# Kernel tuning notes

Measured on AMD Instinct MI355X. Metric: run time of the kernel, lower is better.

## Reference

```python
import jax, jax.numpy as jnp
import numpy as np

D_MODEL = 1024
NUM_HEADS = 16
HEAD_DIM = D_MODEL // NUM_HEADS


def setup_inputs() -> dict:
    key = jax.random.key(0)
    kx, kq, kk, kv, ko = jax.random.split(key, 5)
    B, T = 2, 2048
    scale = 1.0 / np.sqrt(D_MODEL)
    return {
        "x": jax.random.normal(kx, (B, T, D_MODEL), dtype=jnp.float32),
        "wq": jax.random.normal(kq, (D_MODEL, D_MODEL), dtype=jnp.float32) * scale,
        "wk": jax.random.normal(kk, (D_MODEL, D_MODEL), dtype=jnp.float32) * scale,
        "wv": jax.random.normal(kv, (D_MODEL, D_MODEL), dtype=jnp.float32) * scale,
        "wo": jax.random.normal(ko, (D_MODEL, D_MODEL), dtype=jnp.float32) * scale,
    }


def _split_heads(x):
    b, t, _ = x.shape
    return x.reshape(b, t, NUM_HEADS, HEAD_DIM).transpose(0, 2, 1, 3)  # [b,h,t,d]


def reference(x, wq, wk, wv, wo):
    q = _split_heads(x @ wq)
    k = _split_heads(x @ wk)
    v = _split_heads(x @ wv)
    inv_sqrt_d = jnp.asarray(1.0 / np.sqrt(HEAD_DIM), x.dtype)
    scores = jnp.einsum("bhqd,bhkd->bhqk", q, k) * inv_sqrt_d
    weights = jax.nn.softmax(scores, axis=-1)  # dropout rate 0.0 -> identity
    out = jnp.einsum("bhqk,bhkd->bhqd", weights, v)
    b, h, t, d = out.shape
    out = out.transpose(0, 2, 1, 3).reshape(b, t, D_MODEL)
    return out @ wo
```

## Files before the change

### kernel.cpp

```cpp
#include <hip/hip_runtime.h>
#include <stdint.h>

using bf16   = __bf16;
using bf16x8 = __bf16 __attribute__((ext_vector_type(8)));
using bf16x4 = __bf16 __attribute__((ext_vector_type(4)));
using f32x4  = float  __attribute__((ext_vector_type(4)));
using f32x16 = float  __attribute__((ext_vector_type(16)));
using u32x4  = uint32_t __attribute__((ext_vector_type(4)));

#define DM 1024
#define T_ 2048
#define NH 16

__device__ __forceinline__ void gl_lds16(const void* g, void* l) {
  __builtin_amdgcn_global_load_lds(
      (__attribute__((address_space(1))) void*)g,
      (__attribute__((address_space(3))) void*)l, 16, 0, 0);
}

__device__ __forceinline__ f32x4 mfma16(bf16x8 a, bf16x8 b, f32x4 c) {
  return __builtin_amdgcn_mfma_f32_16x16x32_bf16(a, b, c, 0, 0, 0);
}
__device__ __forceinline__ f32x16 mfma32(bf16x8 a, bf16x8 b, f32x16 c) {
  return __builtin_amdgcn_mfma_f32_32x32x16_bf16(a, b, c, 0, 0, 0);
}
__device__ __forceinline__ uint32_t cvtpk(float lo, float hi) {
  uint32_t r;
  asm volatile("v_cvt_pk_bf16_f32 %0, %1, %2" : "=v"(r) : "v"(lo), "v"(hi));
  return r;
}

__global__ __launch_bounds__(256)
void k_prep(const float* __restrict__ x,
            const float* __restrict__ w0, const float* __restrict__ w1,
            const float* __restrict__ w2, const float* __restrict__ w3,
            bf16* __restrict__ xb, bf16* __restrict__ wtq, bf16* __restrict__ wto) {
  __shared__ float tile[64][68];
  const int bid = blockIdx.x;
  if (bid < 2048) {
    const size_t i = (size_t)bid * 256 + threadIdx.x;
    const float4 a = *(const float4*)(x + i * 8);
    const float4 c = *(const float4*)(x + i * 8 + 4);
    bf16x8 v;
    v[0] = (bf16)a.x; v[1] = (bf16)a.y; v[2] = (bf16)a.z; v[3] = (bf16)a.w;
    v[4] = (bf16)c.x; v[5] = (bf16)c.y; v[6] = (bf16)c.z; v[7] = (bf16)c.w;
    *(bf16x8*)(xb + i * 8) = v;
    return;
  }
  const int wblk = bid - 2048;
  const int z = wblk >> 8;
  const int bx = wblk & 15, by = (wblk >> 4) & 15;
  const float* w = (z == 0) ? w0 : (z == 1) ? w1 : (z == 2) ? w2 : w3;
  bf16* wt = (z < 3) ? (wtq + (size_t)z * 1024 * 1024) : wto;
  const float scale = (z == 0) ? 0.125f * 1.44269504f : 1.0f;
  const int tx = threadIdx.x & 15;
  const int ty = threadIdx.x >> 4;
  const int k0 = by * 64, n0 = bx * 64;
#pragma unroll
  for (int j = 0; j < 4; ++j) {
    const int r = ty + 16 * j;
    const float4 v = *(const float4*)(w + (size_t)(k0 + r) * DM + n0 + tx * 4);
    tile[r][tx * 4 + 0] = v.x; tile[r][tx * 4 + 1] = v.y;
    tile[r][tx * 4 + 2] = v.z; tile[r][tx * 4 + 3] = v.w;
  }
  __syncthreads();
#pragma unroll
  for (int j = 0; j < 4; ++j) {
    const int r = ty + 16 * j;
    bf16x4 o;
    o[0] = (bf16)(tile[tx * 4 + 0][r] * scale);
    o[1] = (bf16)(tile[tx * 4 + 1][r] * scale);
    o[2] = (bf16)(tile[tx * 4 + 2][r] * scale);
    o[3] = (bf16)(tile[tx * 4 + 3][r] * scale);
    *(bf16x4*)(wt + (size_t)(n0 + r) * DM + k0 + tx * 4) = o;
  }
}

template<int MODE>
__global__ __launch_bounds__(256)
void k_gemm(const bf16* __restrict__ A, const bf16* __restrict__ BT,
            bf16* __restrict__ Qg, bf16* __restrict__ Kf, bf16* __restrict__ Vf,
            float* __restrict__ Cout) {
  constexpr int BN = (MODE == 0) ? 128 : 64;
  constexpr int NTW = BN / 32;
  constexpr int TNX = (MODE == 0) ? 3 : 2;
  __shared__ __align__(16) bf16 Ash[128 * 32];
  __shared__ __align__(16) bf16 Bsh[BN * 32];
  const int xcd = blockIdx.x & 7, idx = blockIdx.x >> 3;
  const int tn = xcd * TNX + idx % TNX;
  const int tm = idx / TNX;
  const int lane = threadIdx.x & 63, w = threadIdx.x >> 6;
  const int wm = w >> 1, wn = w & 1;
  const int r16 = lane & 15, g = lane >> 4;
  f32x4 acc[4][NTW] = {};
  const bf16* Arow = A + (size_t)tm * 128 * DM;
  const bf16* Brow = BT + (size_t)tn * BN * DM;
  for (int k0 = 0; k0 < DM; k0 += 32) {
#pragma unroll
    for (int t = 0; t < 2; ++t) {
      const int q = t * 256 + w * 64 + lane;
      gl_lds16(Arow + (size_t)(q >> 2) * DM + k0 + (q & 3) * 8, Ash + (t * 256 + w * 64) * 8);
    }
#pragma unroll
    for (int t = 0; t < BN / 64; ++t) {
      const int q = t * 256 + w * 64 + lane;
      gl_lds16(Brow + (size_t)(q >> 2) * DM + k0 + (q & 3) * 8, Bsh + (t * 256 + w * 64) * 8);
    }
    __syncthreads();
    bf16x8 af[4], bfr[NTW];
#pragma unroll
    for (int mt = 0; mt < 4; ++mt)
      af[mt] = *(const bf16x8*)(Ash + (wm * 64 + mt * 16 + r16) * 32 + g * 8);
#pragma unroll
    for (int nt = 0; nt < NTW; ++nt)
      bfr[nt] = *(const bf16x8*)(Bsh + (wn * (BN / 2) + nt * 16 + r16) * 32 + g * 8);
#pragma unroll
    for (int mt = 0; mt < 4; ++mt)
#pragma unroll
      for (int nt = 0; nt < NTW; ++nt)
        acc[mt][nt] = mfma16(af[mt], bfr[nt], acc[mt][nt]);
    __syncthreads();
  }
#pragma unroll
  for (int mt = 0; mt < 4; ++mt) {
#pragma unroll
    for (int nt = 0; nt < NTW; ++nt) {
      const int ncol = tn * BN + wn * (BN / 2) + nt * 16 + r16;
      const int m0 = tm * 128 + wm * 64 + mt * 16 + g * 4;
      if (MODE == 0) {
        const int which = ncol >> 10, nl = ncol & 1023;
        const int h = nl >> 6, d = nl & 63;
        const int b = m0 >> 11, t0 = m0 & 2047;
        const size_t hb = (size_t)(b * NH + h) * (T_ * 64);
        if (which == 2) {
          const int kt = t0 >> 6, s = (t0 & 63) >> 4, hi2 = (t0 >> 3) & 1, j0 = t0 & 7;
          const int dh = d >> 5, d31 = d & 31;
          bf16x4 pv;
#pragma unroll
          for (int r = 0; r < 4; ++r) pv[r] = (bf16)acc[mt][nt][r];
          *(bf16x4*)(Vf + hb + kt * 4096 + (s * 2 + dh) * 512 + (hi2 * 32 + d31) * 8 + j0) = pv;
        } else if (which == 1) {
          const int kt = t0 >> 6, kh2 = (t0 >> 5) & 1;
          const int s = d >> 4, hi2 = (d >> 3) & 1, j = d & 7;
          bf16* base = Kf + hb + kt * 4096 + (s * 2 + kh2) * 512 + hi2 * 256 + j;
#pragma unroll
          for (int r = 0; r < 4; ++r)
            base[((t0 & 31) + r) * 8] = (bf16)acc[mt][nt][r];
        } else {
#pragma unroll
          for (int r = 0; r < 4; ++r)
            Qg[hb + (size_t)(t0 + r) * 64 + d] = (bf16)acc[mt][nt][r];
        }
      } else {
#pragma unroll
        for (int r = 0; r < 4; ++r)
          Cout[(size_t)(m0 + r) * DM + ncol] = acc[mt][nt][r];
      }
    }
  }
}

__global__ __launch_bounds__(512)
void k_attn(const bf16* __restrict__ Qg, const bf16* __restrict__ Kf,
            const bf16* __restrict__ Vf, bf16* __restrict__ Ao) {
  __shared__ __align__(16) bf16 Ksh[2][2][64 * 64];
  __shared__ __align__(16) bf16 Vsh[2][2][64 * 64];
  __shared__ float Lsh[4][64];
  const int lin = ((blockIdx.x & 7) << 6) | (blockIdx.x >> 3);
  const int bh = lin >> 4, qt = lin & 15;
  const int lane = threadIdx.x & 63, w = threadIdx.x >> 6;
  const int qw = w & 3, kh = w >> 2;
  const int l31 = lane & 31, hi = lane >> 5;
  const bf16* Qb  = Qg + (size_t)bh * T_ * 64;
  const bf16* Kfh = Kf + (size_t)bh * T_ * 64;
  const bf16* Vfh = Vf + (size_t)bh * T_ * 64;
  const int q0 = qt * 128 + qw * 32;
  bf16x8 qb[4];
#pragma unroll
  for (int s = 0; s < 4; ++s)
    qb[s] = *(const bf16x8*)(Qb + (size_t)(q0 + l31) * 64 + s * 16 + hi * 8);
  f32x16 o0 = {}, o1 = {};
  float llocal = 0.f;

  auto stage = [&](int buf, int ti) {
#pragma unroll
    for (int j = 0; j < 2; ++j) {
      const int idx = qw * 2 + j;
      gl_lds16(Kfh + (size_t)ti * 4096 + idx * 512 + lane * 8, &Ksh[kh][buf][idx * 512]);
      gl_lds16(Vfh + (size_t)ti * 4096 + idx * 512 + lane * 8, &Vsh[kh][buf][idx * 512]);
    }
  };
  auto pvstep = [&](const f32x16& sv, int si, const bf16* Vc, int s) {
    uint32_t a0 = cvtpk(sv[si + 0], sv[si + 1]);
    uint32_t a1 = cvtpk(sv[si + 2], sv[si + 3]);
    uint32_t b0 = cvtpk(sv[si + 4], sv[si + 5]);
    uint32_t b1 = cvtpk(sv[si + 6], sv[si + 7]);
    asm volatile("v_permlane32_swap_b32 %0, %1" : "+v"(a0), "+v"(b0));
    asm volatile("v_permlane32_swap_b32 %0, %1" : "+v"(a1), "+v"(b1));
    u32x4 fr; fr[0] = a0; fr[1] = a1; fr[2] = b0; fr[3] = b1;
    const bf16x8 pas = __builtin_bit_cast(bf16x8, fr);
    const bf16x8 v0 = *(const bf16x8*)(Vc + (s * 2 + 0) * 512 + lane * 8);
    const bf16x8 v1 = *(const bf16x8*)(Vc + (s * 2 + 1) * 512 + lane * 8);
    o0 = mfma32(pas, v0, o0);
    o1 = mfma32(pas, v1, o1);
  };

  constexpr int NTH = T_ / 64 / 2;
  stage(0, kh * NTH);
  __syncthreads();
  for (int i = 0; i < NTH; ++i) {
    const int cur = i & 1;
    if (i + 1 < NTH) stage(cur ^ 1, kh * NTH + i + 1);
    const bf16* Kc = &Ksh[kh][cur][0];
    const bf16* Vc = &Vsh[kh][cur][0];
    f32x16 st0 = {}, st1 = {};
    __builtin_amdgcn_s_setprio(1);
#pragma unroll
    for (int s = 0; s < 4; ++s) {
      const bf16x8 k0 = *(const bf16x8*)(Kc + (s * 2 + 0) * 512 + lane * 8);
      st0 = mfma32(k0, qb[s], st0);
    }
#pragma unroll
    for (int s = 0; s < 4; ++s) {
      const bf16x8 k1 = *(const bf16x8*)(Kc + (s * 2 + 1) * 512 + lane * 8);
      st1 = mfma32(k1, qb[s], st1);
    }
    __builtin_amdgcn_s_setprio(0);
#pragma unroll
    for (int r = 0; r < 16; ++r) {
      st0[r] = __builtin_amdgcn_exp2f(st0[r]); llocal += st0[r];
    }
    __builtin_amdgcn_s_setprio(1);
    pvstep(st0, 0, Vc, 0);
    pvstep(st0, 8, Vc, 1);
    __builtin_amdgcn_s_setprio(0);
#pragma unroll
    for (int r = 0; r < 16; ++r) {
      st1[r] = __builtin_amdgcn_exp2f(st1[r]); llocal += st1[r];
    }
    __builtin_amdgcn_s_setprio(1);
    pvstep(st1, 0, Vc, 2);
    pvstep(st1, 8, Vc, 3);
    __builtin_amdgcn_s_setprio(0);
    __syncthreads();
  }
  float* cb = (float*)&Ksh[0][0][0] + qw * 2048;
  if (kh == 1) {
#pragma unroll
    for (int r = 0; r < 16; ++r) {
      cb[r * 64 + lane]        = o0[r];
      cb[(16 + r) * 64 + lane] = o1[r];
    }
    Lsh[qw][lane] = llocal;
  }
  __syncthreads();
  if (kh == 0) {
    llocal += Lsh[qw][lane];
#pragma unroll
    for (int r = 0; r < 16; ++r) {
      o0[r] += cb[r * 64 + lane];
      o1[r] += cb[(16 + r) * 64 + lane];
    }
    llocal += __shfl_xor(llocal, 32);
    const int b = bh >> 4, h = bh & 15;
#pragma unroll
    for (int r = 0; r < 16; ++r) {
      const int qoff = (r & 3) + 8 * (r >> 2) + 4 * hi;
      const float linv = 1.f / __shfl(llocal, qoff);
      const size_t base = ((size_t)(b * T_ + q0 + qoff)) * DM + h * 64 + l31;
      Ao[base]      = (bf16)(o0[r] * linv);
      Ao[base + 32] = (bf16)(o1[r] * linv);
    }
  }
}

extern "C" void kernel_launch(void* const* d_in, const int* in_sizes, int n_in,
                              void* d_out, int out_size, void* d_ws, size_t ws_size,
                              hipStream_t stream) {
  const float* x  = (const float*)d_in[0];
  const float* wq = (const float*)d_in[1];
  const float* wk = (const float*)d_in[2];
  const float* wv = (const float*)d_in[3];
  const float* wo = (const float*)d_in[4];
  char* ws = (char*)d_ws;
  const size_t MB = 1024 * 1024;
  bf16* xb   = (bf16*)(ws + 0);
  bf16* wtq  = (bf16*)(ws + 8 * MB);
  bf16* wto  = (bf16*)(ws + 14 * MB);
  bf16* Qg   = (bf16*)(ws + 16 * MB);
  bf16* Kfb  = (bf16*)(ws + 24 * MB);
  bf16* Vfb  = (bf16*)(ws + 32 * MB);

  k_prep<<<dim3(3072), dim3(256), 0, stream>>>(x, wq, wk, wv, wo, xb, wtq, wto);
  k_gemm<0><<<dim3(768), dim3(256), 0, stream>>>(xb, wtq, Qg, Kfb, Vfb, (float*)nullptr);
  k_attn<<<dim3(512), dim3(512), 0, stream>>>(Qg, Kfb, Vfb, xb);
  k_gemm<1><<<dim3(512), dim3(256), 0, stream>>>(xb, wto, (bf16*)nullptr, (bf16*)nullptr,
                                                 (bf16*)nullptr, (float*)d_out);
}
```

Before: 119.0 us.

## Double GEMM K-tile to 64 with XOR-swizzled LDS layout

After: 121.6 us. 2.1% more time.

```diff
diff --git a/kernel.cpp b/kernel.cpp
--- a/kernel.cpp
+++ b/kernel.cpp
@@ -84,41 +84,55 @@
   constexpr int BN = (MODE == 0) ? 128 : 64;
   constexpr int NTW = BN / 32;
   constexpr int TNX = (MODE == 0) ? 3 : 2;
-  __shared__ __align__(16) bf16 Ash[128 * 32];
-  __shared__ __align__(16) bf16 Bsh[BN * 32];
+  __shared__ __align__(16) bf16 Ash[128 * 64];
+  __shared__ __align__(16) bf16 Bsh[BN * 64];
   const int xcd = blockIdx.x & 7, idx = blockIdx.x >> 3;
   const int tn = xcd * TNX + idx % TNX;
   const int tm = idx / TNX;
   const int lane = threadIdx.x & 63, w = threadIdx.x >> 6;
   const int wm = w >> 1, wn = w & 1;
   const int r16 = lane & 15, g = lane >> 4;
+  const int srow8 = lane >> 3;
+  const int sch = (lane & 7) ^ srow8;
   f32x4 acc[4][NTW] = {};
   const bf16* Arow = A + (size_t)tm * 128 * DM;
   const bf16* Brow = BT + (size_t)tn * BN * DM;
-  for (int k0 = 0; k0 < DM; k0 += 32) {
-#pragma unroll
-    for (int t = 0; t < 2; ++t) {
-      const int q = t * 256 + w * 64 + lane;
-      gl_lds16(Arow + (size_t)(q >> 2) * DM + k0 + (q & 3) * 8, Ash + (t * 256 + w * 64) * 8);
-    }
-#pragma unroll
-    for (int t = 0; t < BN / 64; ++t) {
-      const int q = t * 256 + w * 64 + lane;
-      gl_lds16(Brow + (size_t)(q >> 2) * DM + k0 + (q & 3) * 8, Bsh + (t * 256 + w * 64) * 8);
+  for (int k0 = 0; k0 < DM; k0 += 64) {
+#pragma unroll
+    for (int j = 0; j < 4; ++j) {
+      const int rb = w * 32 + j * 8;
+      gl_lds16(Arow + (size_t)(rb + srow8) * DM + k0 + sch * 8, Ash + rb * 64);
+    }
+#pragma unroll
+    for (int j = 0; j < BN / 32; ++j) {
+      const int rb = w * (BN / 4) + j * 8;
+      gl_lds16(Brow + (size_t)(rb + srow8) * DM + k0 + sch * 8, Bsh + rb * 64);
     }
     __syncthreads();
-    bf16x8 af[4], bfr[NTW];
-#pragma unroll
-    for (int mt = 0; mt < 4; ++mt)
-      af[mt] = *(const bf16x8*)(Ash + (wm * 64 + mt * 16 + r16) * 32 + g * 8);
-#pragma unroll
-    for (int nt = 0; nt < NTW; ++nt)
-      bfr[nt] = *(const bf16x8*)(Bsh + (wn * (BN / 2) + nt * 16 + r16) * 32 + g * 8);
-#pragma unroll
-    for (int mt = 0; mt < 4; ++mt)
-#pragma unroll
-      for (int nt = 0; nt < NTW; ++nt)
-        acc[mt][nt] = mfma16(af[mt], bfr[nt], acc[mt][nt]);
+    bf16x8 af[4][2], bfr[NTW][2];
+#pragma unroll
+    for (int mt = 0; mt < 4; ++mt) {
+      const int R = wm * 64 + mt * 16 + r16;
+#pragma unroll
+      for (int kk = 0; kk < 2; ++kk)
+        af[mt][kk] = *(const bf16x8*)((const char*)Ash + R * 128 +
+                                      (((kk * 4 + g) ^ (R & 7)) << 4));
+    }
+#pragma unroll
+    for (int nt = 0; nt < NTW; ++nt) {
+      const int R = wn * (BN / 2) + nt * 16 + r16;
+#pragma unroll
+      for (int kk = 0; kk < 2; ++kk)
+        bfr[nt][kk] = *(const bf16x8*)((const char*)Bsh + R * 128 +
+                                       (((kk * 4 + g) ^ (R & 7)) << 4));
+    }
+#pragma unroll
+    for (int kk = 0; kk < 2; ++kk)
+#pragma unroll
+      for (int mt = 0; mt < 4; ++mt)
+#pragma unroll
+        for (int nt = 0; nt < NTW; ++nt)
+          acc[mt][nt] = mfma16(af[mt][kk], bfr[nt][kk], acc[mt][nt]);
     __syncthreads();
   }
 #pragma unroll
```

## Double-buffer GEMM LDS tiles and split softmax row-sum accumulators

Applied to the files above, without the earlier changes.

Result: slower. 124.3 us (+4.4%).

```diff
diff --git a/kernel.cpp b/kernel.cpp
--- a/kernel.cpp
+++ b/kernel.cpp
@@ -84,8 +84,9 @@
   constexpr int BN = (MODE == 0) ? 128 : 64;
   constexpr int NTW = BN / 32;
   constexpr int TNX = (MODE == 0) ? 3 : 2;
-  __shared__ __align__(16) bf16 Ash[128 * 32];
-  __shared__ __align__(16) bf16 Bsh[BN * 32];
+  constexpr int NKI = DM / 32;
+  __shared__ __align__(16) bf16 Ash[2][128 * 32];
+  __shared__ __align__(16) bf16 Bsh[2][BN * 32];
   const int xcd = blockIdx.x & 7, idx = blockIdx.x >> 3;
   const int tn = xcd * TNX + idx % TNX;
   const int tm = idx / TNX;
@@ -95,25 +96,34 @@
   f32x4 acc[4][NTW] = {};
   const bf16* Arow = A + (size_t)tm * 128 * DM;
   const bf16* Brow = BT + (size_t)tn * BN * DM;
-  for (int k0 = 0; k0 < DM; k0 += 32) {
+
+  auto stage = [&](int buf, int k0) {
 #pragma unroll
     for (int t = 0; t < 2; ++t) {
       const int q = t * 256 + w * 64 + lane;
-      gl_lds16(Arow + (size_t)(q >> 2) * DM + k0 + (q & 3) * 8, Ash + (t * 256 + w * 64) * 8);
+      gl_lds16(Arow + (size_t)(q >> 2) * DM + k0 + (q & 3) * 8,
+               &Ash[buf][(t * 256 + w * 64) * 8]);
     }
 #pragma unroll
     for (int t = 0; t < BN / 64; ++t) {
       const int q = t * 256 + w * 64 + lane;
-      gl_lds16(Brow + (size_t)(q >> 2) * DM + k0 + (q & 3) * 8, Bsh + (t * 256 + w * 64) * 8);
-    }
-    __syncthreads();
+      gl_lds16(Brow + (size_t)(q >> 2) * DM + k0 + (q & 3) * 8,
+               &Bsh[buf][(t * 256 + w * 64) * 8]);
+    }
+  };
+
+  stage(0, 0);
+  __syncthreads();
+  for (int i = 0; i < NKI; ++i) {
+    const int cur = i & 1;
+    if (i + 1 < NKI) stage(cur ^ 1, (i + 1) * 32);
     bf16x8 af[4], bfr[NTW];
 #pragma unroll
     for (int mt = 0; mt < 4; ++mt)
-      af[mt] = *(const bf16x8*)(Ash + (wm * 64 + mt * 16 + r16) * 32 + g * 8);
+      af[mt] = *(const bf16x8*)(&Ash[cur][(wm * 64 + mt * 16 + r16) * 32 + g * 8]);
 #pragma unroll
     for (int nt = 0; nt < NTW; ++nt)
-      bfr[nt] = *(const bf16x8*)(Bsh + (wn * (BN / 2) + nt * 16 + r16) * 32 + g * 8);
+      bfr[nt] = *(const bf16x8*)(&Bsh[cur][(wn * (BN / 2) + nt * 16 + r16) * 32 + g * 8]);
 #pragma unroll
     for (int mt = 0; mt < 4; ++mt)
 #pragma unroll
@@ -180,7 +190,7 @@
   for (int s = 0; s < 4; ++s)
     qb[s] = *(const bf16x8*)(Qb + (size_t)(q0 + l31) * 64 + s * 16 + hi * 8);
   f32x16 o0 = {}, o1 = {};
-  float llocal = 0.f;
+  float lacc0 = 0.f, lacc1 = 0.f, lacc2 = 0.f, lacc3 = 0.f;
 
   auto stage = [&](int buf, int ti) {
 #pragma unroll
@@ -227,16 +237,22 @@
     }
     __builtin_amdgcn_s_setprio(0);
 #pragma unroll
-    for (int r = 0; r < 16; ++r) {
-      st0[r] = __builtin_amdgcn_exp2f(st0[r]); llocal += st0[r];
+    for (int r = 0; r < 16; r += 4) {
+      st0[r + 0] = __builtin_amdgcn_exp2f(st0[r + 0]); lacc0 += st0[r + 0];
+      st0[r + 1] = __builtin_amdgcn_exp2f(st0[r + 1]); lacc1 += st0[r + 1];
+      st0[r + 2] = __builtin_amdgcn_exp2f(st0[r + 2]); lacc2 += st0[r + 2];
+      st0[r + 3] = __builtin_amdgcn_exp2f(st0[r + 3]); lacc3 += st0[r + 3];
     }
     __builtin_amdgcn_s_setprio(1);
     pvstep(st0, 0, Vc, 0);
     pvstep(st0, 8, Vc, 1);
     __builtin_amdgcn_s_setprio(0);
 #pragma unroll
-    for (int r = 0; r < 16; ++r) {
-      st1[r] = __builtin_amdgcn_exp2f(st1[r]); llocal += st1[r];
+    for (int r = 0; r < 16; r += 4) {
+      st1[r + 0] = __builtin_amdgcn_exp2f(st1[r + 0]); lacc0 += st1[r + 0];
+      st1[r + 1] = __builtin_amdgcn_exp2f(st1[r + 1]); lacc1 += st1[r + 1];
+      st1[r + 2] = __builtin_amdgcn_exp2f(st1[r + 2]); lacc2 += st1[r + 2];
+      st1[r + 3] = __builtin_amdgcn_exp2f(st1[r + 3]); lacc3 += st1[r + 3];
     }
     __builtin_amdgcn_s_setprio(1);
     pvstep(st1, 0, Vc, 2);
@@ -244,6 +260,7 @@
     __builtin_amdgcn_s_setprio(0);
     __syncthreads();
   }
+  float llocal = (lacc0 + lacc1) + (lacc2 + lacc3);
   float* cb = (float*)&Ksh[0][0][0] + qw * 2048;
   if (kh == 1) {
 #pragma unroll
```

## Load K/V fragments directly from global into registers, drop LDS staging

Applied to the files above, without the earlier changes.

Result: no change. 121.2 us (+1.9%).

```diff
diff --git a/kernel.cpp b/kernel.cpp
--- a/kernel.cpp
+++ b/kernel.cpp
@@ -163,8 +163,7 @@
 __global__ __launch_bounds__(512)
 void k_attn(const bf16* __restrict__ Qg, const bf16* __restrict__ Kf,
             const bf16* __restrict__ Vf, bf16* __restrict__ Ao) {
-  __shared__ __align__(16) bf16 Ksh[2][2][64 * 64];
-  __shared__ __align__(16) bf16 Vsh[2][2][64 * 64];
+  __shared__ float Csh[4][32 * 64];
   __shared__ float Lsh[4][64];
   const int lin = ((blockIdx.x & 7) << 6) | (blockIdx.x >> 3);
   const int bh = lin >> 4, qt = lin & 15;
@@ -172,25 +171,19 @@
   const int qw = w & 3, kh = w >> 2;
   const int l31 = lane & 31, hi = lane >> 5;
   const bf16* Qb  = Qg + (size_t)bh * T_ * 64;
-  const bf16* Kfh = Kf + (size_t)bh * T_ * 64;
-  const bf16* Vfh = Vf + (size_t)bh * T_ * 64;
   const int q0 = qt * 128 + qw * 32;
   bf16x8 qb[4];
 #pragma unroll
   for (int s = 0; s < 4; ++s)
     qb[s] = *(const bf16x8*)(Qb + (size_t)(q0 + l31) * 64 + s * 16 + hi * 8);
   f32x16 o0 = {}, o1 = {};
-  float llocal = 0.f;
-
-  auto stage = [&](int buf, int ti) {
-#pragma unroll
-    for (int j = 0; j < 2; ++j) {
-      const int idx = qw * 2 + j;
-      gl_lds16(Kfh + (size_t)ti * 4096 + idx * 512 + lane * 8, &Ksh[kh][buf][idx * 512]);
-      gl_lds16(Vfh + (size_t)ti * 4096 + idx * 512 + lane * 8, &Vsh[kh][buf][idx * 512]);
-    }
-  };
-  auto pvstep = [&](const f32x16& sv, int si, const bf16* Vc, int s) {
+  float lacc0 = 0.f, lacc1 = 0.f, lacc2 = 0.f, lacc3 = 0.f;
+
+  constexpr int NTH = T_ / 64 / 2;
+  const bf16* Kt = Kf + (size_t)bh * T_ * 64 + (size_t)(kh * NTH) * 4096 + lane * 8;
+  const bf16* Vt = Vf + (size_t)bh * T_ * 64 + (size_t)(kh * NTH) * 4096 + lane * 8;
+
+  auto pvstep = [&](const f32x16& sv, int si, bf16x8 v0, bf16x8 v1) {
     uint32_t a0 = cvtpk(sv[si + 0], sv[si + 1]);
     uint32_t a1 = cvtpk(sv[si + 2], sv[si + 3]);
     uint32_t b0 = cvtpk(sv[si + 4], sv[si + 5]);
@@ -199,52 +192,51 @@
     asm volatile("v_permlane32_swap_b32 %0, %1" : "+v"(a1), "+v"(b1));
     u32x4 fr; fr[0] = a0; fr[1] = a1; fr[2] = b0; fr[3] = b1;
     const bf16x8 pas = __builtin_bit_cast(bf16x8, fr);
-    const bf16x8 v0 = *(const bf16x8*)(Vc + (s * 2 + 0) * 512 + lane * 8);
-    const bf16x8 v1 = *(const bf16x8*)(Vc + (s * 2 + 1) * 512 + lane * 8);
     o0 = mfma32(pas, v0, o0);
     o1 = mfma32(pas, v1, o1);
   };
 
-  constexpr int NTH = T_ / 64 / 2;
-  stage(0, kh * NTH);
-  __syncthreads();
+#pragma unroll 1
   for (int i = 0; i < NTH; ++i) {
-    const int cur = i & 1;
-    if (i + 1 < NTH) stage(cur ^ 1, kh * NTH + i + 1);
-    const bf16* Kc = &Ksh[kh][cur][0];
-    const bf16* Vc = &Vsh[kh][cur][0];
+    const bf16* kp = Kt + (size_t)i * 4096;
+    bf16x8 kf[8];
+#pragma unroll
+    for (int u = 0; u < 8; ++u) kf[u] = *(const bf16x8*)(kp + u * 512);
     f32x16 st0 = {}, st1 = {};
     __builtin_amdgcn_s_setprio(1);
 #pragma unroll
     for (int s = 0; s < 4; ++s) {
-      const bf16x8 k0 = *(const bf16x8*)(Kc + (s * 2 + 0) * 512 + lane * 8);
-      st0 = mfma32(k0, qb[s], st0);
-    }
-#pragma unroll
-    for (int s = 0; s < 4; ++s) {
-      const bf16x8 k1 = *(const bf16x8*)(Kc + (s * 2 + 1) * 512 + lane * 8);
-      st1 = mfma32(k1, qb[s], st1);
+      st0 = mfma32(kf[s * 2 + 0], qb[s], st0);
+      st1 = mfma32(kf[s * 2 + 1], qb[s], st1);
     }
     __builtin_amdgcn_s_setprio(0);
-#pragma unroll
-    for (int r = 0; r < 16; ++r) {
-      st0[r] = __builtin_amdgcn_exp2f(st0[r]); llocal += st0[r];
+    const bf16* vp = Vt + (size_t)i * 4096;
+    bf16x8 vf[8];
+#pragma unroll
+    for (int u = 0; u < 8; ++u) vf[u] = *(const bf16x8*)(vp + u * 512);
+#pragma unroll
+    for (int r = 0; r < 16; r += 4) {
+      st0[r + 0] = __builtin_amdgcn_exp2f(st0[r + 0]); lacc0 += st0[r + 0];
+      st0[r + 1] = __builtin_amdgcn_exp2f(st0[r + 1]); lacc1 += st0[r + 1];
+      st0[r + 2] = __builtin_amdgcn_exp2f(st0[r + 2]); lacc2 += st0[r + 2];
+      st0[r + 3] = __builtin_amdgcn_exp2f(st0[r + 3]); lacc3 += st0[r + 3];
+    }
+#pragma unroll
+    for (int r = 0; r < 16; r += 4) {
+      st1[r + 0] = __builtin_amdgcn_exp2f(st1[r + 0]); lacc0 += st1[r + 0];
+      st1[r + 1] = __builtin_amdgcn_exp2f(st1[r + 1]); lacc1 += st1[r + 1];
+      st1[r + 2] = __builtin_amdgcn_exp2f(st1[r + 2]); lacc2 += st1[r + 2];
+      st1[r + 3] = __builtin_amdgcn_exp2f(st1[r + 3]); lacc3 += st1[r + 3];
     }
     __builtin_amdgcn_s_setprio(1);
-    pvstep(st0, 0, Vc, 0);
-    pvstep(st0, 8, Vc, 1);
+    pvstep(st0, 0, vf[0], vf[1]);
+    pvstep(st0, 8, vf[2], vf[3]);
+    pvstep(st1, 0, vf[4], vf[5]);
+    pvstep(st1, 8, vf[6], vf[7]);
     __builtin_amdgcn_s_setprio(0);
-#pragma unroll
-    for (int r = 0; r < 16; ++r) {
-      st1[r] = __builtin_amdgcn_exp2f(st1[r]); llocal += st1[r];
-    }
-    __builtin_amdgcn_s_setprio(1);
-    pvstep(st1, 0, Vc, 2);
-    pvstep(st1, 8, Vc, 3);
-    __builtin_amdgcn_s_setprio(0);
-    __syncthreads();
-  }
-  float* cb = (float*)&Ksh[0][0][0] + qw * 2048;
+  }
+  float llocal = (lacc0 + lacc1) + (lacc2 + lacc3);
+  float* cb = &Csh[qw][0];
   if (kh == 1) {
 #pragma unroll
     for (int r = 0; r < 16; ++r) {
```
